# Kernel optimization log

Hardware: AMD Instinct MI355X
Metric: run time of the kernel (lower is better)

The kernel has to match this reference:

```python
import jax, jax.numpy as jnp
import numpy as np

# locally-connected conv constants (match init_kwargs)
SH, SW = 2, 2      # stride
KH, KW = 8, 8      # kernel dims
PH, PW = 0, 0      # padding


def setup_inputs() -> dict:
    key = jax.random.key(0)
    k1, k2 = jax.random.split(key)
    x = jax.random.normal(k1, (16, 3, 128, 128), dtype=jnp.float32)
    # untied weights: one [OC, C, KH, KW] filter per output location (61x61 grid)
    W = jax.random.normal(k2, (61, 61, 64, 3, 8, 8), dtype=jnp.float32) * 0.05
    bias = jnp.zeros((64, 61, 61), dtype=jnp.float32)
    return {"x": x, "W": W, "bias": bias}


def reference(x, W, bias):
    B = x.shape[0]
    NH, NW, OC = W.shape[0], W.shape[1], W.shape[2]
    xp = jnp.pad(x, ((0, 0), (0, 0), (PH, PH), (PW, PW)))
    # gather all patches at once: rows[NH,KH], cols[NW,KW]
    rows = (jnp.arange(NH) * SH)[:, None] + jnp.arange(KH)
    cols = (jnp.arange(NW) * SW)[:, None] + jnp.arange(KW)
    # patches: [B, C, NH, NW, KH, KW]
    patches = xp[:, :, rows[:, None, :, None], cols[None, :, None, :]]
    # per-location matmul (untied conv): out [B, OC, NH, NW]
    out = jnp.einsum('bchwij,hwocij->bohw', patches, W) + bias[None]
    # flatten_into_2D: interleave sqrt(OC) x sqrt(OC) channel blocks into spatial map
    r = int(np.sqrt(OC))  # 8
    o = out.transpose(0, 2, 3, 1).reshape(B, NH, NW, r, r)
    o = o.transpose(0, 1, 3, 2, 4).reshape(B, r * NH, r * NW)
    return o[:, None]  # [B, 1, r*NH, r*NW]
```

## Files before the change

### kernel.cpp

```cpp
#include <hip/hip_runtime.h>


namespace {
constexpr int NHW  = 61 * 61;
constexpr int XB   = 3 * 128 * 128;
constexpr int XCC  = 128 * 128;
constexpr int OSTR = 488 * 488;
}

typedef __fp16   fp16x2 __attribute__((ext_vector_type(2)));
typedef _Float16 half8v __attribute__((ext_vector_type(8)));
typedef float    f32x4  __attribute__((ext_vector_type(4)));

union H8 { fp16x2 p[4]; half8v h; uint4 u; };

__global__ __launch_bounds__(256, 5) void lc2d_kernel(
    const float* __restrict__ xg,
    const float* __restrict__ wg,
    const float* __restrict__ bg,
    float* __restrict__ og)
{
    __shared__ __align__(16) _Float16 wlh[64 * 192];
    __shared__ __align__(16) _Float16 xlh[16 * 192];

    const int hw   = blockIdx.x;
    const int h    = hw / 61;
    const int w    = hw - h * 61;
    const int t    = threadIdx.x;
    const int lane = t & 63;
    const int wv   = t >> 6;

    const float* wbase = wg + (size_t)hw * (64 * 192);
    const float* xb    = xg + (h * 2) * 128 + (w * 2);

    float4 wr[12];
    #pragma unroll
    for (int it = 0; it < 6; ++it) {
        const int g  = it * 256 + t;
        const int oc = g / 24;
        const int s8 = g - oc * 24;
        const float* src = wbase + oc * 192 + s8 * 8;
        wr[it * 2]     = *reinterpret_cast<const float4*>(src);
        wr[it * 2 + 1] = *reinterpret_cast<const float4*>(src + 4);
    }
    float2 xr[6];
    #pragma unroll
    for (int it = 0; it < 6; ++it) {
        const int f  = it * 256 + t;
        const int b  = f / 96;
        const int r  = f - b * 96;
        const int k  = r * 2;
        const int c  = k >> 6;
        const int i  = (k >> 3) & 7;
        const int j  = k & 7;
        xr[it] = *reinterpret_cast<const float2*>(xb + b * XB + c * XCC + i * 128 + j);
    }
    __builtin_amdgcn_sched_barrier(0);

    #pragma unroll
    for (int it = 0; it < 6; ++it) {
        const int g  = it * 256 + t;
        const int oc = g / 24;
        const int s8 = g - oc * 24;
        H8 u;
        u.p[0] = __builtin_amdgcn_cvt_pkrtz(wr[it*2].x,   wr[it*2].y);
        u.p[1] = __builtin_amdgcn_cvt_pkrtz(wr[it*2].z,   wr[it*2].w);
        u.p[2] = __builtin_amdgcn_cvt_pkrtz(wr[it*2+1].x, wr[it*2+1].y);
        u.p[3] = __builtin_amdgcn_cvt_pkrtz(wr[it*2+1].z, wr[it*2+1].w);
        int srot = s8 + (oc & 7); if (srot >= 24) srot -= 24;
        *reinterpret_cast<uint4*>(&wlh[oc * 192 + srot * 8]) = u.u;
    }
    #pragma unroll
    for (int it = 0; it < 6; ++it) {
        const int f  = it * 256 + t;
        const int b  = f / 96;
        const int r  = f - b * 96;
        const int s8 = r >> 2;
        const int j  = (r & 3) * 2;
        const fp16x2 pk = __builtin_amdgcn_cvt_pkrtz(xr[it].x, xr[it].y);
        int srot = s8 + (b & 7); if (srot >= 24) srot -= 24;
        union { fp16x2 p; unsigned u; } cv; cv.p = pk;
        *reinterpret_cast<unsigned*>(&xlh[b * 192 + srot * 8 + j]) = cv.u;
    }
    __syncthreads();

    const int lq  = lane & 15;
    const int lk  = lane >> 4;
    const int ocl = wv * 16 + lq;

    f32x4 acc = {0.f, 0.f, 0.f, 0.f};
    #pragma unroll
    for (int ks = 0; ks < 6; ++ks) {
        const int slog = ks * 4 + lk;
        int sa = slog + (lq & 7);   if (sa >= 24) sa -= 24;
        int sb = slog + (ocl & 7);  if (sb >= 24) sb -= 24;
        const half8v av = *reinterpret_cast<const half8v*>(&xlh[lq  * 192 + sa * 8]);
        const half8v bv = *reinterpret_cast<const half8v*>(&wlh[ocl * 192 + sb * 8]);
        acc = __builtin_amdgcn_mfma_f32_16x16x32_f16(av, bv, acc, 0, 0, 0);
    }

    const float bz = bg[ocl * NHW + hw];
    float* ob = og + (h * 8 + (ocl >> 3)) * 488 + (w * 8 + (ocl & 7));
    #pragma unroll
    for (int r = 0; r < 4; ++r) {
        const int b = lk * 4 + r;
        ob[(size_t)b * OSTR] = acc[r] + bz;
    }
}

extern "C" void kernel_launch(void* const* d_in, const int* in_sizes, int n_in,
                              void* d_out, int out_size, void* d_ws, size_t ws_size,
                              hipStream_t stream) {
    const float* x    = (const float*)d_in[0];
    const float* W    = (const float*)d_in[1];
    const float* bias = (const float*)d_in[2];
    float* out        = (float*)d_out;
    lc2d_kernel<<<dim3(NHW), dim3(256), 0, stream>>>(x, W, bias, out);
}
```

Measured before the change: 39.66 us.

## Convert to persistent grid with register double-buffered prefetch of next tile

```diff
diff --git a/kernel.cpp b/kernel.cpp
--- a/kernel.cpp
+++ b/kernel.cpp
@@ -6,6 +6,7 @@
 constexpr int XB   = 3 * 128 * 128;
 constexpr int XCC  = 128 * 128;
 constexpr int OSTR = 488 * 488;
+constexpr int GRID = 512;
 }
 
 typedef __fp16   fp16x2 __attribute__((ext_vector_type(2)));
@@ -14,97 +15,140 @@
 
 union H8 { fp16x2 p[4]; half8v h; uint4 u; };
 
-__global__ __launch_bounds__(256, 5) void lc2d_kernel(
+__global__ __launch_bounds__(256, 2) void lc2d_kernel(
     const float* __restrict__ xg,
     const float* __restrict__ wg,
     const float* __restrict__ bg,
     float* __restrict__ og)
 {
-    __shared__ __align__(16) _Float16 wlh[64 * 192];
-    __shared__ __align__(16) _Float16 xlh[16 * 192];
+    __shared__ __align__(16) _Float16 wlh[2][64 * 192];
+    __shared__ __align__(16) _Float16 xlh[2][16 * 192];
 
-    const int hw   = blockIdx.x;
-    const int h    = hw / 61;
-    const int w    = hw - h * 61;
+    const int bid  = blockIdx.x;
     const int t    = threadIdx.x;
     const int lane = t & 63;
     const int wv   = t >> 6;
+    const int lq   = lane & 15;
+    const int lk   = lane >> 4;
+    const int ocl  = wv * 16 + lq;
+    const int nt   = 7 + (bid < (NHW - 7 * GRID));
 
-    const float* wbase = wg + (size_t)hw * (64 * 192);
-    const float* xb    = xg + (h * 2) * 128 + (w * 2);
+    auto issue = [&](float4 (&wr)[12], float2 (&xr)[6], float& bz, int hw)
+        __attribute__((always_inline)) {
+        const float* wbase = wg + (size_t)hw * 12288;
+        #pragma unroll
+        for (int it = 0; it < 6; ++it) {
+            const int g  = it * 256 + t;
+            const int oc = g / 24;
+            const int s8 = g - oc * 24;
+            const float* src = wbase + oc * 192 + s8 * 8;
+            wr[it * 2]     = *reinterpret_cast<const float4*>(src);
+            wr[it * 2 + 1] = *reinterpret_cast<const float4*>(src + 4);
+        }
+        const int hh = hw / 61;
+        const int ww = hw - hh * 61;
+        const float* xb = xg + hh * 2 * 128 + ww * 2;
+        #pragma unroll
+        for (int it = 0; it < 6; ++it) {
+            const int f  = it * 256 + t;
+            const int b  = f / 96;
+            const int r  = f - b * 96;
+            const int k  = r * 2;
+            const int c  = k >> 6;
+            const int ii = (k >> 3) & 7;
+            const int j  = k & 7;
+            xr[it] = *reinterpret_cast<const float2*>(xb + b * XB + c * XCC + ii * 128 + j);
+        }
+        bz = bg[ocl * NHW + hw];
+    };
 
-    float4 wr[12];
-    #pragma unroll
-    for (int it = 0; it < 6; ++it) {
-        const int g  = it * 256 + t;
-        const int oc = g / 24;
-        const int s8 = g - oc * 24;
-        const float* src = wbase + oc * 192 + s8 * 8;
-        wr[it * 2]     = *reinterpret_cast<const float4*>(src);
-        wr[it * 2 + 1] = *reinterpret_cast<const float4*>(src + 4);
-    }
-    float2 xr[6];
-    #pragma unroll
-    for (int it = 0; it < 6; ++it) {
-        const int f  = it * 256 + t;
-        const int b  = f / 96;
-        const int r  = f - b * 96;
-        const int k  = r * 2;
-        const int c  = k >> 6;
-        const int i  = (k >> 3) & 7;
-        const int j  = k & 7;
-        xr[it] = *reinterpret_cast<const float2*>(xb + b * XB + c * XCC + i * 128 + j);
-    }
-    __builtin_amdgcn_sched_barrier(0);
+    auto convw = [&](float4 (&wr)[12], float2 (&xr)[6], int p)
+        __attribute__((always_inline)) {
+        #pragma unroll
+        for (int it = 0; it < 6; ++it) {
+            const int g  = it * 256 + t;
+            const int oc = g / 24;
+            const int s8 = g - oc * 24;
+            H8 u;
+            u.p[0] = __builtin_amdgcn_cvt_pkrtz(wr[it*2].x,   wr[it*2].y);
+            u.p[1] = __builtin_amdgcn_cvt_pkrtz(wr[it*2].z,   wr[it*2].w);
+            u.p[2] = __builtin_amdgcn_cvt_pkrtz(wr[it*2+1].x, wr[it*2+1].y);
+            u.p[3] = __builtin_amdgcn_cvt_pkrtz(wr[it*2+1].z, wr[it*2+1].w);
+            int srot = s8 + (oc & 7); if (srot >= 24) srot -= 24;
+            *reinterpret_cast<uint4*>(&wlh[p][oc * 192 + srot * 8]) = u.u;
+        }
+        #pragma unroll
+        for (int it = 0; it < 6; ++it) {
+            const int f  = it * 256 + t;
+            const int b  = f / 96;
+            const int r  = f - b * 96;
+            const int s8 = r >> 2;
+            const int j  = (r & 3) * 2;
+            const fp16x2 pk = __builtin_amdgcn_cvt_pkrtz(xr[it].x, xr[it].y);
+            int srot = s8 + (b & 7); if (srot >= 24) srot -= 24;
+            union { fp16x2 pp; unsigned u; } cv; cv.pp = pk;
+            *reinterpret_cast<unsigned*>(&xlh[p][b * 192 + srot * 8 + j]) = cv.u;
+        }
+    };
 
-    #pragma unroll
-    for (int it = 0; it < 6; ++it) {
-        const int g  = it * 256 + t;
-        const int oc = g / 24;
-        const int s8 = g - oc * 24;
-        H8 u;
-        u.p[0] = __builtin_amdgcn_cvt_pkrtz(wr[it*2].x,   wr[it*2].y);
-        u.p[1] = __builtin_amdgcn_cvt_pkrtz(wr[it*2].z,   wr[it*2].w);
-        u.p[2] = __builtin_amdgcn_cvt_pkrtz(wr[it*2+1].x, wr[it*2+1].y);
-        u.p[3] = __builtin_amdgcn_cvt_pkrtz(wr[it*2+1].z, wr[it*2+1].w);
-        int srot = s8 + (oc & 7); if (srot >= 24) srot -= 24;
-        *reinterpret_cast<uint4*>(&wlh[oc * 192 + srot * 8]) = u.u;
-    }
-    #pragma unroll
-    for (int it = 0; it < 6; ++it) {
-        const int f  = it * 256 + t;
-        const int b  = f / 96;
-        const int r  = f - b * 96;
-        const int s8 = r >> 2;
-        const int j  = (r & 3) * 2;
-        const fp16x2 pk = __builtin_amdgcn_cvt_pkrtz(xr[it].x, xr[it].y);
-        int srot = s8 + (b & 7); if (srot >= 24) srot -= 24;
-        union { fp16x2 p; unsigned u; } cv; cv.p = pk;
-        *reinterpret_cast<unsigned*>(&xlh[b * 192 + srot * 8 + j]) = cv.u;
-    }
-    __syncthreads();
+    auto compute = [&](int p, float bz, int hw) __attribute__((always_inline)) {
+        const int hh = hw / 61;
+        const int ww = hw - hh * 61;
+        f32x4 acc = {0.f, 0.f, 0.f, 0.f};
+        #pragma unroll
+        for (int ks = 0; ks < 6; ++ks) {
+            const int slog = ks * 4 + lk;
+            int sa = slog + (lq & 7);  if (sa >= 24) sa -= 24;
+            int sb = slog + (ocl & 7); if (sb >= 24) sb -= 24;
+            const half8v av = *reinterpret_cast<const half8v*>(&xlh[p][lq  * 192 + sa * 8]);
+            const half8v bv = *reinterpret_cast<const half8v*>(&wlh[p][ocl * 192 + sb * 8]);
+            acc = __builtin_amdgcn_mfma_f32_16x16x32_f16(av, bv, acc, 0, 0, 0);
+        }
+        float* ob = og + (hh * 8 + (ocl >> 3)) * 488 + (ww * 8 + (ocl & 7));
+        #pragma unroll
+        for (int r = 0; r < 4; ++r) {
+            const int b = lk * 4 + r;
+            ob[(size_t)b * OSTR] = acc[r] + bz;
+        }
+    };
 
-    const int lq  = lane & 15;
-    const int lk  = lane >> 4;
-    const int ocl = wv * 16 + lq;
+    float4 wrA[12], wrB[12];
+    float2 xrA[6],  xrB[6];
+    float  bzA = 0.f, bzB = 0.f;
 
-    f32x4 acc = {0.f, 0.f, 0.f, 0.f};
-    #pragma unroll
-    for (int ks = 0; ks < 6; ++ks) {
-        const int slog = ks * 4 + lk;
-        int sa = slog + (lq & 7);   if (sa >= 24) sa -= 24;
-        int sb = slog + (ocl & 7);  if (sb >= 24) sb -= 24;
-        const half8v av = *reinterpret_cast<const half8v*>(&xlh[lq  * 192 + sa * 8]);
-        const half8v bv = *reinterpret_cast<const half8v*>(&wlh[ocl * 192 + sb * 8]);
-        acc = __builtin_amdgcn_mfma_f32_16x16x32_f16(av, bv, acc, 0, 0, 0);
-    }
-
-    const float bz = bg[ocl * NHW + hw];
-    float* ob = og + (h * 8 + (ocl >> 3)) * 488 + (w * 8 + (ocl & 7));
-    #pragma unroll
-    for (int r = 0; r < 4; ++r) {
-        const int b = lk * 4 + r;
-        ob[(size_t)b * OSTR] = acc[r] + bz;
+    issue(wrA, xrA, bzA, bid);
+    int i = 0;
+    while (true) {
+        {
+            if (i + 1 < nt) {
+                issue(wrB, xrB, bzB, bid + (i + 1) * GRID);
+                asm volatile("s_waitcnt vmcnt(19)" ::: "memory");
+            } else {
+                asm volatile("s_waitcnt vmcnt(4)" ::: "memory");
+            }
+            __builtin_amdgcn_sched_barrier(0);
+            convw(wrA, xrA, i & 1);
+            asm volatile("s_waitcnt lgkmcnt(0)" ::: "memory");
+            __builtin_amdgcn_s_barrier();
+            __builtin_amdgcn_sched_barrier(0);
+            compute(i & 1, bzA, bid + i * GRID);
+            ++i; if (i >= nt) break;
+        }
+        {
+            if (i + 1 < nt) {
+                issue(wrA, xrA, bzA, bid + (i + 1) * GRID);
+                asm volatile("s_waitcnt vmcnt(19)" ::: "memory");
+            } else {
+                asm volatile("s_waitcnt vmcnt(4)" ::: "memory");
+            }
+            __builtin_amdgcn_sched_barrier(0);
+            convw(wrB, xrB, i & 1);
+            asm volatile("s_waitcnt lgkmcnt(0)" ::: "memory");
+            __builtin_amdgcn_s_barrier();
+            __builtin_amdgcn_sched_barrier(0);
+            compute(i & 1, bzB, bid + i * GRID);
+            ++i; if (i >= nt) break;
+        }
     }
 }
 
@@ -115,5 +159,5 @@
     const float* W    = (const float*)d_in[1];
     const float* bias = (const float*)d_in[2];
     float* out        = (float*)d_out;
-    lc2d_kernel<<<dim3(NHW), dim3(256), 0, stream>>>(x, W, bias, out);
+    lc2d_kernel<<<dim3(GRID), dim3(256), 0, stream>>>(x, W, bias, out);
 }
```

Measured after the change: 42.63 us. 1.07x slower.
